# Kernel optimization log

Measured on AMD Instinct MI355X. Metric: run time of the kernel, lower is better.

## Reference

```python
import jax, jax.numpy as jnp
import numpy as np

N = 100_000      # nodes
E = 500_000      # bonds
DN = 128         # dim_node_embedding
DB = 64          # dim_bond_embedding
NTOK = 4         # num_bond_token
DIN = 2 * DN + 2 * DB  # 384
LEAKY = 0.001
LN_EPS = 1e-5
DIST_MAX = 20.0
STEP = 0.5


def _lrelu(v):
    return jnp.where(v >= 0, v, LEAKY * v)


def _layernorm(v, w, b):
    m = v.mean(-1, keepdims=True)
    var = ((v - m) ** 2).mean(-1, keepdims=True)
    return (v - m) / jnp.sqrt(var + LN_EPS) * w + b


def setup_inputs() -> dict:
    key = jax.random.key(0)
    ks = jax.random.split(key, 20)
    x = jax.random.normal(ks[0], (N, 3), dtype=jnp.float32) * 3.0
    pos = jax.random.normal(ks[1], (N, 3), dtype=jnp.float32)
    node_embedding = jax.random.normal(ks[2], (N, DN), dtype=jnp.float32)
    i0 = jax.random.randint(ks[3], (E,), 0, N)
    off = jax.random.randint(ks[4], (E,), 1, N)  # nonzero -> no self-bonds
    bond_index = jnp.stack([i0, (i0 + off) % N], axis=1).astype(jnp.int32)
    bond_types = jax.random.randint(ks[5], (E,), 0, NTOK).astype(jnp.int32)
    s = 0.02
    params = dict(
        bond_emb=jax.random.normal(ks[6], (NTOK, DB), dtype=jnp.float32),
        W0=jax.random.normal(ks[7], (DIN, DN), dtype=jnp.float32) * s,
        b0=jnp.zeros((DN,), jnp.float32),
        W1=jax.random.normal(ks[8], (DN, DN), dtype=jnp.float32) * s,
        b1=jnp.zeros((DN,), jnp.float32),
        ln1_w=jnp.ones((DN,), jnp.float32),
        ln1_b=jnp.zeros((DN,), jnp.float32),
        W2=jax.random.normal(ks[9], (DN, DN), dtype=jnp.float32) * s,
        b2=jnp.zeros((DN,), jnp.float32),
        ln2_w=jnp.ones((DN,), jnp.float32),
        ln2_b=jnp.zeros((DN,), jnp.float32),
        Wo=jax.random.normal(ks[10], (DN, 2), dtype=jnp.float32) * s,
        bo=jnp.zeros((2,), jnp.float32),
    )
    return dict(x=x, pos=pos, node_embedding=node_embedding,
                bond_index=bond_index, bond_types=bond_types, **params)


def reference(x, pos, node_embedding, bond_index, bond_types,
              bond_emb, W0, b0, W1, b1, ln1_w, ln1_b,
              W2, b2, ln2_w, ln2_b, Wo, bo):
    i = bond_index[:, 0]
    j = bond_index[:, 1]

    # ---- BondLength geometry ----
    diff = x[i] - x[j]                                   # [E,3]
    dist = jnp.linalg.norm(diff, axis=-1, keepdims=True)  # [E,1]
    u = diff / dist                                       # [E,3] unit j->i? (i-j)/d
    direction = jnp.stack([u, -u], axis=-1)               # [E,3,2]

    # ---- Smearing (gaussian RBF + overflow bin, normalized) ----
    offset = jnp.linspace(0.0, DIST_MAX, DB - 1, dtype=jnp.float32)  # [63]
    delta = DIST_MAX / (DB - 2)
    coeff = -0.5 / (delta * delta)
    rbf = jnp.exp(coeff * (dist - offset) ** 2)            # [E,63]
    ovf = (dist >= DIST_MAX).astype(x.dtype)               # [E,1]
    smear = jnp.concatenate([rbf, ovf], axis=-1)           # [E,64]
    smear = smear / smear.sum(axis=-1, keepdims=True)

    # ---- Edge MLP (LeakyMLP, num_layer=2, dim_end=2) ----
    feat = jnp.concatenate(
        [node_embedding[i], node_embedding[j], bond_emb[bond_types], smear],
        axis=-1)                                           # [E,384]
    h = _lrelu(feat @ W0 + b0)
    h = _lrelu(_layernorm(h @ W1 + b1, ln1_w, ln1_b))
    h = _lrelu(_layernorm(h @ W2 + b2, ln2_w, ln2_b))
    force = h @ Wo + bo                                    # [E,2]

    # ---- position update (scatter-add) ----
    update = force[:, None, :] * direction                 # [E,3,2]
    pos = pos.at[i].add(STEP * update[..., 0])
    pos = pos.at[j].add(STEP * update[..., 1])
    return pos
```

## Files before the change

kernel.cpp:

```cpp
#include <hip/hip_runtime.h>
#include <stdint.h>

#define N_EDGES 500000
#define N_NODES 100000
#define PREP_NG 2
#define TBINS 1280

typedef __attribute__((ext_vector_type(8))) short short8;
typedef __attribute__((ext_vector_type(4))) float floatx4;
typedef __attribute__((ext_vector_type(2))) float f32x2;

__device__ __forceinline__ uint16_t f2bf(float f) {
  union { float f; uint32_t u; } cv; cv.f = f;
  uint32_t u = cv.u;
  return (uint16_t)((u + 0x7FFFu + ((u >> 16) & 1u)) >> 16);
}
__device__ __forceinline__ uint32_t pk2bf(float lo, float hi) {
  return __builtin_amdgcn_perm(__float_as_uint(hi), __float_as_uint(lo), 0x07060302u);
}
__device__ __forceinline__ uint16_t bftrunc(float f) {
  return (uint16_t)(__float_as_uint(f) >> 16);
}
__device__ __forceinline__ float lrelu(float v) { return fmaxf(v, 0.001f * v); }

__device__ __forceinline__ f32x2 unpk2(uint32_t u) {
  return (f32x2){ __uint_as_float(u << 16), __uint_as_float(u & 0xFFFF0000u) };
}
__device__ __forceinline__ uint32_t comp2(uint32_t a, uint32_t b, uint32_t t0, uint32_t t1,
                                          f32x2 w2) {
  f32x2 p  = unpk2(a) + unpk2(b);
  f32x2 v0 = unpk2(t0), v1 = unpk2(t1);
  f32x2 r  = p + (v0 + w2 * (v1 - v0));
  f32x2 rl = r * 0.001f;
  return pk2bf(fmaxf(r.x, rl.x), fmaxf(r.y, rl.y));
}
__device__ __forceinline__ floatx4 lrelu4(floatx4 v) {
  floatx4 w = v * 0.001f;
  v.x = fmaxf(v.x, w.x); v.y = fmaxf(v.y, w.y);
  v.z = fmaxf(v.z, w.z); v.w = fmaxf(v.w, w.w);
  return v;
}

__global__ void prep0_kernel(const float* __restrict__ W0, const float* __restrict__ b0,
                             const float* __restrict__ W1, const float* __restrict__ W2,
                             const float* __restrict__ bemb,
                             uint16_t* __restrict__ w0ab, uint16_t* __restrict__ w1f,
                             uint16_t* __restrict__ w2f, float* __restrict__ be0f,
                             const float* __restrict__ pos, float* __restrict__ out, int npos) {
  int id = blockIdx.x * 256 + threadIdx.x;
  if (id < 32768) {
    int f = id;
    int j = f & 7, lane = (f >> 3) & 63, ntt = (f >> 9) & 15, ks = f >> 13;
    int k = ks * 32 + (lane >> 4) * 8 + j;
    int row = (ntt < 8) ? k : (128 + k);
    int col = (ntt & 7) * 16 + (lane & 15);
    w0ab[f] = f2bf(W0[row * 128 + col]);
  } else if (id < 49152) {
    int f = id - 32768;
    int j = f & 7, lane = (f >> 3) & 63, nt = (f >> 9) & 7, ks = f >> 12;
    int k = ks * 32 + (lane >> 4) * 8 + j;
    w1f[f] = f2bf(W1[k * 128 + nt * 16 + (lane & 15)]);
  } else if (id < 65536) {
    int f = id - 49152;
    int j = f & 7, lane = (f >> 3) & 63, nt = (f >> 9) & 7, ks = f >> 12;
    int k = ks * 32 + (lane >> 4) * 8 + j;
    w2f[f] = f2bf(W2[k * 128 + nt * 16 + (lane & 15)]);
  } else if (id < 66048) {
    int t = id - 65536; int ty = t >> 7, n = t & 127;
    float s = b0[n];
    for (int kk = 0; kk < 64; ++kk) s += bemb[ty * 64 + kk] * W0[(256 + kk) * 128 + n];
    be0f[t] = s;
  } else if (id - 66048 < npos) {
    out[id - 66048] = pos[id - 66048];
  }
}

__global__ __attribute__((amdgpu_flat_work_group_size(256, 256)))
void prep_tp_kernel(const float* __restrict__ W0, const float* __restrict__ be0f,
                    uint16_t* __restrict__ T,
                    const float* __restrict__ nemb, const uint16_t* __restrict__ w0ab,
                    uint16_t* __restrict__ Pa, uint16_t* __restrict__ Pb) {
  __shared__ __align__(16) uint16_t aLds[4 * PREP_NG * 16 * 136];
  __shared__ __align__(16) uint16_t sS[4][16][72];
  __shared__ float rbf[64];
  const int tid = threadIdx.x;

  if (blockIdx.x < TBINS) {
    int b = blockIdx.x;
    float dist = (float)b * (1.0f / 32.0f);
    const float delta = 20.0f / 62.0f;
    const float coeff = -0.5f / (delta * delta);
    if (tid < 64) {
      float v;
      if (tid < 63) { float d = dist - (float)tid * delta; v = __expf(coeff * d * d); }
      else v = (dist >= 20.0f) ? 1.0f : 0.0f;
      rbf[tid] = v;
    }
    __syncthreads();
    float sum = 0.0f;
    for (int k = 0; k < 64; ++k) sum += rbf[k];
    float rs = 1.0f / sum;
    for (int o = tid; o < 512; o += 256) {
      int ty = o >> 7, n = o & 127;
      float s = be0f[ty * 128 + n];
      for (int k = 0; k < 64; ++k) s += rbf[k] * rs * W0[(320 + k) * 128 + n];
      T[((size_t)(ty * TBINS + b)) * 128 + n] = f2bf(s);
    }
    return;
  }

  const int pblk = blockIdx.x - TBINS;
  const int lane = tid & 63;
  const int wave = tid >> 6;
  const int n15 = lane & 15;
  const int quad = lane >> 4;
  uint16_t* myA = aLds + wave * (PREP_NG * 16 * 136);
  const int base = pblk * (64 * PREP_NG) + wave * (16 * PREP_NG);

  {
    const int le = lane >> 2, sub = lane & 3;
#pragma unroll
    for (int it = 0; it < PREP_NG; ++it) {
      int r = base + it * 16 + le; if (r >= N_NODES) r = N_NODES - 1;
      const float4* src = (const float4*)(nemb + (size_t)r * 128);
#pragma unroll
      for (int g = 0; g < 4; ++g) {
        float4 a = src[sub * 8 + g * 2], b = src[sub * 8 + g * 2 + 1];
        uint4 pk;
        pk.x = pk2bf(a.x, a.y); pk.y = pk2bf(a.z, a.w);
        pk.z = pk2bf(b.x, b.y); pk.w = pk2bf(b.z, b.w);
        *(uint4*)(myA + (it * 16 + le) * 136 + sub * 32 + g * 8) = pk;
      }
    }
  }

  const short8* wfv = (const short8*)w0ab + lane;
  const int srow = lane >> 2, sch = lane & 3;
#pragma unroll
  for (int q = 0; q < 4; ++q) {
    short8 bfr[16];
#pragma unroll
    for (int ks = 0; ks < 4; ++ks)
#pragma unroll
      for (int nq = 0; nq < 4; ++nq)
        bfr[ks * 4 + nq] = wfv[(ks * 16 + q * 4 + nq) * 64];
    uint16_t* dst = (q < 2) ? Pa : Pb;
    const int cbase = (q & 1) * 64;
#pragma unroll
    for (int it = 0; it < PREP_NG; ++it) {
      floatx4 acc[4];
#pragma unroll
      for (int nq = 0; nq < 4; ++nq) acc[nq] = (floatx4){0.f, 0.f, 0.f, 0.f};
#pragma unroll
      for (int ks = 0; ks < 4; ++ks) {
        short8 a = *(const short8*)(myA + (it * 16 + n15) * 136 + ks * 32 + quad * 8);
#pragma unroll
        for (int nq = 0; nq < 4; ++nq)
          acc[nq] = __builtin_amdgcn_mfma_f32_16x16x32_bf16(a, bfr[ks * 4 + nq], acc[nq], 0, 0, 0);
      }
#pragma unroll
      for (int nq = 0; nq < 4; ++nq)
#pragma unroll
        for (int r = 0; r < 4; ++r)
          sS[wave][quad * 4 + r][nq * 16 + n15] = bftrunc(acc[nq][r]);
      int grow = base + it * 16 + srow;
      if (grow < N_NODES) {
        uint16_t* drow = dst + (size_t)grow * 128 + cbase;
#pragma unroll
        for (int h = 0; h < 2; ++h)
          *(uint4*)(drow + (h * 4 + sch) * 8) =
              *(const uint4*)&sS[wave][srow][(h * 4 + sch) * 8];
      }
    }
  }
}

__device__ __forceinline__ void gemm_g2(const uint16_t* __restrict__ wf,
                                        const uint16_t* aRow0, const uint16_t* aRow1,
                                        int lane, floatx4* acc0, floatx4* acc1) {
  short8 a0[4], a1[4];
#pragma unroll
  for (int ks = 0; ks < 4; ++ks) {
    a0[ks] = *(const short8*)(aRow0 + ks * 32);
    a1[ks] = *(const short8*)(aRow1 + ks * 32);
  }
  const short8* wv = (const short8*)wf + lane;
#pragma unroll
  for (int ks = 0; ks < 4; ++ks)
#pragma unroll
    for (int nt = 0; nt < 8; ++nt) {
      short8 b = wv[(ks * 8 + nt) * 64];
      acc0[nt] = __builtin_amdgcn_mfma_f32_16x16x32_bf16(a0[ks], b, acc0[nt], 0, 0, 0);
      acc1[nt] = __builtin_amdgcn_mfma_f32_16x16x32_bf16(a1[ks], b, acc1[nt], 0, 0, 0);
    }
}

__device__ __forceinline__ void epilogue1(floatx4* acc, uint16_t* hA, int n15, int quad,
                                          const float* __restrict__ b1,
                                          const float* __restrict__ ln1w,
                                          const float* __restrict__ ln1b) {
  float bv[8], wv[8], bb[8];
#pragma unroll
  for (int nt = 0; nt < 8; ++nt) {
    int col = nt * 16 + n15;
    bv[nt] = b1[col]; wv[nt] = ln1w[col]; bb[nt] = ln1b[col];
  }
  floatx4 s4 = {0.f, 0.f, 0.f, 0.f}, q4 = {0.f, 0.f, 0.f, 0.f};
#pragma unroll
  for (int nt = 0; nt < 8; ++nt) { floatx4 v = acc[nt] + bv[nt]; s4 += v; q4 += v * v; }
#pragma unroll
  for (int m = 1; m <= 8; m <<= 1) {
#pragma unroll
    for (int c = 0; c < 4; ++c) { s4[c] += __shfl_xor(s4[c], m); q4[c] += __shfl_xor(q4[c], m); }
  }
  floatx4 mean = s4 * (1.0f / 128.0f);
  floatx4 var = q4 * (1.0f / 128.0f) - mean * mean;
  floatx4 rstd;
  rstd.x = rsqrtf(var.x + 1e-5f); rstd.y = rsqrtf(var.y + 1e-5f);
  rstd.z = rsqrtf(var.z + 1e-5f); rstd.w = rsqrtf(var.w + 1e-5f);
#pragma unroll
  for (int nt = 0; nt < 8; ++nt) {
    floatx4 v = acc[nt] + bv[nt];
    floatx4 vn = lrelu4((v - mean) * (rstd * wv[nt]) + bb[nt]);
#pragma unroll
    for (int r = 0; r < 4; ++r)
      hA[(quad * 4 + r) * 136 + nt * 16 + n15] = bftrunc(vn[r]);
  }
}

__device__ __forceinline__ void epilogue2(floatx4* acc, int n15, int quad, int edge0, int gr0,
                                          const float (*u_lds)[3], const int (*ij_lds)[2],
                                          const float* __restrict__ b2,
                                          const float* __restrict__ ln2w,
                                          const float* __restrict__ ln2b,
                                          const float* __restrict__ Wo,
                                          const float* __restrict__ bo,
                                          float* __restrict__ out) {
  float bv[8], wv[8], bb[8], wo0[8], wo1[8];
#pragma unroll
  for (int nt = 0; nt < 8; ++nt) {
    int col = nt * 16 + n15;
    bv[nt] = b2[col]; wv[nt] = ln2w[col]; bb[nt] = ln2b[col];
    wo0[nt] = Wo[2 * col]; wo1[nt] = Wo[2 * col + 1];
  }
  floatx4 s4 = {0.f, 0.f, 0.f, 0.f}, q4 = {0.f, 0.f, 0.f, 0.f};
#pragma unroll
  for (int nt = 0; nt < 8; ++nt) { floatx4 v = acc[nt] + bv[nt]; s4 += v; q4 += v * v; }
#pragma unroll
  for (int m = 1; m <= 8; m <<= 1) {
#pragma unroll
    for (int c = 0; c < 4; ++c) { s4[c] += __shfl_xor(s4[c], m); q4[c] += __shfl_xor(q4[c], m); }
  }
  floatx4 mean = s4 * (1.0f / 128.0f);
  floatx4 var = q4 * (1.0f / 128.0f) - mean * mean;
  floatx4 rstd;
  rstd.x = rsqrtf(var.x + 1e-5f); rstd.y = rsqrtf(var.y + 1e-5f);
  rstd.z = rsqrtf(var.z + 1e-5f); rstd.w = rsqrtf(var.w + 1e-5f);
  floatx4 f0 = {0.f, 0.f, 0.f, 0.f}, f1 = {0.f, 0.f, 0.f, 0.f};
#pragma unroll
  for (int nt = 0; nt < 8; ++nt) {
    floatx4 v = acc[nt] + bv[nt];
    floatx4 vn = lrelu4((v - mean) * (rstd * wv[nt]) + bb[nt]);
    f0 += vn * wo0[nt];
    f1 += vn * wo1[nt];
  }
#pragma unroll
  for (int m = 1; m <= 8; m <<= 1) {
#pragma unroll
    for (int c = 0; c < 4; ++c) { f0[c] += __shfl_xor(f0[c], m); f1[c] += __shfl_xor(f1[c], m); }
  }
  if (n15 < 4) {
    int gr = gr0 + quad * 4 + n15;
    int ge2 = edge0 + quad * 4 + n15;
    if (ge2 < N_EDGES) {
      float F0 = (n15 == 0) ? f0.x : (n15 == 1) ? f0.y : (n15 == 2) ? f0.z : f0.w;
      float F1 = (n15 == 0) ? f1.x : (n15 == 1) ? f1.y : (n15 == 2) ? f1.z : f1.w;
      F0 += bo[0]; F1 += bo[1];
      float ux = u_lds[gr][0], uy = u_lds[gr][1], uz = u_lds[gr][2];
      int ii = ij_lds[gr][0], jj = ij_lds[gr][1];
      float c0 = 0.5f * F0;
      float c1 = -0.5f * F1;
      atomicAdd(out + 3 * ii,     c0 * ux);
      atomicAdd(out + 3 * ii + 1, c0 * uy);
      atomicAdd(out + 3 * ii + 2, c0 * uz);
      atomicAdd(out + 3 * jj,     c1 * ux);
      atomicAdd(out + 3 * jj + 1, c1 * uy);
      atomicAdd(out + 3 * jj + 2, c1 * uz);
    }
  }
}

__global__ __attribute__((amdgpu_flat_work_group_size(256, 256), amdgpu_waves_per_eu(4)))
void bond_mlp_kernel(const float* __restrict__ x,
                     const int* __restrict__ bidx, const int* __restrict__ btyp,
                     const uint16_t* __restrict__ Pa, const uint16_t* __restrict__ Pb,
                     const uint16_t* __restrict__ Tt, const uint16_t* __restrict__ w1f,
                     const uint16_t* __restrict__ w2f,
                     const float* __restrict__ b1, const float* __restrict__ ln1w,
                     const float* __restrict__ ln1b,
                     const float* __restrict__ b2, const float* __restrict__ ln2w,
                     const float* __restrict__ ln2b,
                     const float* __restrict__ Wo, const float* __restrict__ bo,
                     float* __restrict__ out) {
  __shared__ __align__(16) uint16_t hA_all[8 * 16 * 136];
  __shared__ float u_lds[128][3];
  __shared__ int ij_lds[128][2];

  const int tid = threadIdx.x;
  const int lane = tid & 63;
  const int wave = tid >> 6;
  const int n15 = lane & 15;
  const int quad = lane >> 4;

  uint16_t* hA0 = hA_all + (wave * 2 + 0) * (16 * 136);
  uint16_t* hA1 = hA_all + (wave * 2 + 1) * (16 * 136);

#pragma unroll
  for (int g = 0; g < 2; ++g) {
    uint16_t* hA = (g == 0) ? hA0 : hA1;
    const int le = lane >> 2, sub = lane & 3;
    const int gr = wave * 32 + g * 16 + le;
    const int ge = blockIdx.x * 128 + gr;
    const bool valid = ge < N_EDGES;
    int vi = 0, vj = 0, bt = 0;
    if (valid) {
      int2 ij = *(const int2*)(bidx + 2 * ge);
      vi = ij.x; vj = ij.y;
      bt = btyp[ge];
    }
    float dx, dy, dz;
    if (valid) {
      dx = x[3 * vi]     - x[3 * vj];
      dy = x[3 * vi + 1] - x[3 * vj + 1];
      dz = x[3 * vi + 2] - x[3 * vj + 2];
    } else { dx = 1.0f; dy = 0.0f; dz = 0.0f; }
    float dist = sqrtf(dx * dx + dy * dy + dz * dz);
    float rinv = 1.0f / dist;
    if (sub == 0) {
      u_lds[gr][0] = dx * rinv; u_lds[gr][1] = dy * rinv; u_lds[gr][2] = dz * rinv;
      ij_lds[gr][0] = vi; ij_lds[gr][1] = vj;
    }
    float fb = fminf(dist, 39.5f) * 32.0f;
    int bi = (int)fb;
    float w = fb - (float)bi;
    f32x2 w2 = {w, w};
    const uint4* pa = (const uint4*)(Pa + (size_t)vi * 128 + sub * 32);
    const uint4* pb = (const uint4*)(Pb + (size_t)vj * 128 + sub * 32);
    const uint16_t* trow = Tt + ((size_t)(bt * TBINS + bi)) * 128 + sub * 32;
    const uint4* t0p = (const uint4*)trow;
    const uint4* t1p = (const uint4*)(trow + 128);
#pragma unroll
    for (int gg = 0; gg < 4; ++gg) {
      uint4 av = pa[gg], bv = pb[gg], t0 = t0p[gg], t1 = t1p[gg];
      uint4 pk;
      pk.x = comp2(av.x, bv.x, t0.x, t1.x, w2);
      pk.y = comp2(av.y, bv.y, t0.y, t1.y, w2);
      pk.z = comp2(av.z, bv.z, t0.z, t1.z, w2);
      pk.w = comp2(av.w, bv.w, t0.w, t1.w, w2);
      *(uint4*)(hA + le * 136 + sub * 32 + gg * 8) = pk;
    }
  }

  const uint16_t* aRow0 = hA0 + n15 * 136 + quad * 8;
  const uint16_t* aRow1 = hA1 + n15 * 136 + quad * 8;

  floatx4 acc0[8], acc1[8];
#pragma unroll
  for (int nt = 0; nt < 8; ++nt) {
    acc0[nt] = (floatx4){0.f, 0.f, 0.f, 0.f};
    acc1[nt] = (floatx4){0.f, 0.f, 0.f, 0.f};
  }
  gemm_g2(w1f, aRow0, aRow1, lane, acc0, acc1);

  epilogue1(acc0, hA0, n15, quad, b1, ln1w, ln1b);
  epilogue1(acc1, hA1, n15, quad, b1, ln1w, ln1b);

#pragma unroll
  for (int nt = 0; nt < 8; ++nt) {
    acc0[nt] = (floatx4){0.f, 0.f, 0.f, 0.f};
    acc1[nt] = (floatx4){0.f, 0.f, 0.f, 0.f};
  }
  gemm_g2(w2f, aRow0, aRow1, lane, acc0, acc1);

  const int e0 = blockIdx.x * 128 + wave * 32;
  epilogue2(acc0, n15, quad, e0,      wave * 32,      u_lds, ij_lds, b2, ln2w, ln2b, Wo, bo, out);
  epilogue2(acc1, n15, quad, e0 + 16, wave * 32 + 16, u_lds, ij_lds, b2, ln2w, ln2b, Wo, bo, out);
}

extern "C" void kernel_launch(void* const* d_in, const int* in_sizes, int n_in,
                              void* d_out, int out_size, void* d_ws, size_t ws_size,
                              hipStream_t stream) {
  const float* x    = (const float*)d_in[0];
  const float* pos  = (const float*)d_in[1];
  const float* nemb = (const float*)d_in[2];
  const int*   bidx = (const int*)d_in[3];
  const int*   btyp = (const int*)d_in[4];
  const float* bemb = (const float*)d_in[5];
  const float* W0   = (const float*)d_in[6];
  const float* b0   = (const float*)d_in[7];
  const float* W1   = (const float*)d_in[8];
  const float* b1   = (const float*)d_in[9];
  const float* ln1w = (const float*)d_in[10];
  const float* ln1b = (const float*)d_in[11];
  const float* W2   = (const float*)d_in[12];
  const float* b2   = (const float*)d_in[13];
  const float* ln2w = (const float*)d_in[14];
  const float* ln2b = (const float*)d_in[15];
  const float* Wo   = (const float*)d_in[16];
  const float* bo   = (const float*)d_in[17];
  float* out = (float*)d_out;

  uint16_t* w0ab = (uint16_t*)d_ws;
  uint16_t* w1f  = w0ab + 32768;
  uint16_t* w2f  = w1f + 16384;
  float*    be0f = (float*)(w2f + 16384);
  uint16_t* Tt   = (uint16_t*)(be0f + 512);
  uint16_t* Pa   = Tt + (size_t)4 * TBINS * 128;
  uint16_t* Pb   = Pa + (size_t)N_NODES * 128;

  const int nblkP = (N_NODES + 64 * PREP_NG - 1) / (64 * PREP_NG);

  prep0_kernel<<<(66048 + out_size + 255) / 256, 256, 0, stream>>>(
      W0, b0, W1, W2, bemb, w0ab, w1f, w2f, be0f, pos, out, out_size);
  prep_tp_kernel<<<TBINS + nblkP, 256, 0, stream>>>(
      W0, be0f, Tt, nemb, w0ab, Pa, Pb);
  bond_mlp_kernel<<<(N_EDGES + 127) / 128, 256, 0, stream>>>(
      x, bidx, btyp, Pa, Pb, Tt, w1f, w2f,
      b1, ln1w, ln1b, b2, ln2w, ln2b, Wo, bo, out);
}
```

Baseline: 367.6 us.

## Process edge groups one at a time and batch gather loads before compute

The gather phase is moved into a helper that issues all node-embedding, table and position loads up front (position as a float3 load) before the interpolation math, which raises memory-level parallelism. The GEMMs now run on one 16-row group at a time with a single accumulator set instead of two interleaved ones, so fewer registers are live. Each weight fragment is then read twice from global/L2 instead of being shared across two MFMAs. The waves-per-EU hint drops from 4 to 3, which gives each wave more registers at the cost of fewer resident waves.

New measurement: 476.6 us. +29.6%, slower.

```diff
diff --git a/kernel.cpp b/kernel.cpp
--- a/kernel.cpp
+++ b/kernel.cpp
@@ -175,24 +175,76 @@
   }
 }
 
-__device__ __forceinline__ void gemm_g2(const uint16_t* __restrict__ wf,
-                                        const uint16_t* aRow0, const uint16_t* aRow1,
-                                        int lane, floatx4* acc0, floatx4* acc1) {
-  short8 a0[4], a1[4];
-#pragma unroll
-  for (int ks = 0; ks < 4; ++ks) {
-    a0[ks] = *(const short8*)(aRow0 + ks * 32);
-    a1[ks] = *(const short8*)(aRow1 + ks * 32);
-  }
+__device__ __forceinline__ void phase1(
+    int ge0, int gr0, int lane,
+    const float* __restrict__ x, const int* __restrict__ bidx,
+    const int* __restrict__ btyp,
+    const uint16_t* __restrict__ Pa, const uint16_t* __restrict__ Pb,
+    const uint16_t* __restrict__ Tt,
+    uint16_t* __restrict__ hA, float (*u_lds)[3], int (*ij_lds)[2]) {
+  const int le = lane >> 2, sub = lane & 3;
+  const int gr = gr0 + le;
+  const int ge = ge0 + le;
+  const bool valid = ge < N_EDGES;
+  int vi = 0, vj = 0, bt = 0;
+  if (valid) {
+    int2 ij = *(const int2*)(bidx + 2 * ge);
+    vi = ij.x; vj = ij.y;
+    bt = btyp[ge];
+  }
+  const uint4* pa = (const uint4*)(Pa + (size_t)vi * 128 + sub * 32);
+  const uint4* pb = (const uint4*)(Pb + (size_t)vj * 128 + sub * 32);
+  uint4 A[4], B[4];
+#pragma unroll
+  for (int g = 0; g < 4; ++g) A[g] = pa[g];
+#pragma unroll
+  for (int g = 0; g < 4; ++g) B[g] = pb[g];
+  float dx, dy, dz;
+  if (valid) {
+    float3 xi = *(const float3*)(x + 3 * vi);
+    float3 xj = *(const float3*)(x + 3 * vj);
+    dx = xi.x - xj.x; dy = xi.y - xj.y; dz = xi.z - xj.z;
+  } else { dx = 1.0f; dy = 0.0f; dz = 0.0f; }
+  float dist = sqrtf(dx * dx + dy * dy + dz * dz);
+  float rinv = 1.0f / dist;
+  if (sub == 0) {
+    u_lds[gr][0] = dx * rinv; u_lds[gr][1] = dy * rinv; u_lds[gr][2] = dz * rinv;
+    ij_lds[gr][0] = vi; ij_lds[gr][1] = vj;
+  }
+  float fb = fminf(dist, 39.5f) * 32.0f;
+  int bi = (int)fb;
+  float w = fb - (float)bi;
+  f32x2 w2 = {w, w};
+  const uint16_t* trow = Tt + ((size_t)(bt * TBINS + bi)) * 128 + sub * 32;
+  const uint4* t0p = (const uint4*)trow;
+  const uint4* t1p = (const uint4*)(trow + 128);
+  uint4 T0[4], T1[4];
+#pragma unroll
+  for (int g = 0; g < 4; ++g) T0[g] = t0p[g];
+#pragma unroll
+  for (int g = 0; g < 4; ++g) T1[g] = t1p[g];
+#pragma unroll
+  for (int g = 0; g < 4; ++g) {
+    uint4 pk;
+    pk.x = comp2(A[g].x, B[g].x, T0[g].x, T1[g].x, w2);
+    pk.y = comp2(A[g].y, B[g].y, T0[g].y, T1[g].y, w2);
+    pk.z = comp2(A[g].z, B[g].z, T0[g].z, T1[g].z, w2);
+    pk.w = comp2(A[g].w, B[g].w, T0[g].w, T1[g].w, w2);
+    *(uint4*)(hA + le * 136 + sub * 32 + g * 8) = pk;
+  }
+}
+
+__device__ __forceinline__ void gemm_g(const uint16_t* __restrict__ wf, const uint16_t* aRow,
+                                       int lane, floatx4* acc) {
+  short8 a[4];
+#pragma unroll
+  for (int ks = 0; ks < 4; ++ks) a[ks] = *(const short8*)(aRow + ks * 32);
   const short8* wv = (const short8*)wf + lane;
 #pragma unroll
   for (int ks = 0; ks < 4; ++ks)
 #pragma unroll
-    for (int nt = 0; nt < 8; ++nt) {
-      short8 b = wv[(ks * 8 + nt) * 64];
-      acc0[nt] = __builtin_amdgcn_mfma_f32_16x16x32_bf16(a0[ks], b, acc0[nt], 0, 0, 0);
-      acc1[nt] = __builtin_amdgcn_mfma_f32_16x16x32_bf16(a1[ks], b, acc1[nt], 0, 0, 0);
-    }
+    for (int nt = 0; nt < 8; ++nt)
+      acc[nt] = __builtin_amdgcn_mfma_f32_16x16x32_bf16(a[ks], wv[(ks * 8 + nt) * 64], acc[nt], 0, 0, 0);
 }
 
 __device__ __forceinline__ void epilogue1(floatx4* acc, uint16_t* hA, int n15, int quad,
@@ -290,7 +342,7 @@
   }
 }
 
-__global__ __attribute__((amdgpu_flat_work_group_size(256, 256), amdgpu_waves_per_eu(4)))
+__global__ __attribute__((amdgpu_flat_work_group_size(256, 256), amdgpu_waves_per_eu(3)))
 void bond_mlp_kernel(const float* __restrict__ x,
                      const int* __restrict__ bidx, const int* __restrict__ btyp,
                      const uint16_t* __restrict__ Pa, const uint16_t* __restrict__ Pb,
@@ -315,76 +367,36 @@
   uint16_t* hA0 = hA_all + (wave * 2 + 0) * (16 * 136);
   uint16_t* hA1 = hA_all + (wave * 2 + 1) * (16 * 136);
 
-#pragma unroll
-  for (int g = 0; g < 2; ++g) {
-    uint16_t* hA = (g == 0) ? hA0 : hA1;
-    const int le = lane >> 2, sub = lane & 3;
-    const int gr = wave * 32 + g * 16 + le;
-    const int ge = blockIdx.x * 128 + gr;
-    const bool valid = ge < N_EDGES;
-    int vi = 0, vj = 0, bt = 0;
-    if (valid) {
-      int2 ij = *(const int2*)(bidx + 2 * ge);
-      vi = ij.x; vj = ij.y;
-      bt = btyp[ge];
-    }
-    float dx, dy, dz;
-    if (valid) {
-      dx = x[3 * vi]     - x[3 * vj];
-      dy = x[3 * vi + 1] - x[3 * vj + 1];
-      dz = x[3 * vi + 2] - x[3 * vj + 2];
-    } else { dx = 1.0f; dy = 0.0f; dz = 0.0f; }
-    float dist = sqrtf(dx * dx + dy * dy + dz * dz);
-    float rinv = 1.0f / dist;
-    if (sub == 0) {
-      u_lds[gr][0] = dx * rinv; u_lds[gr][1] = dy * rinv; u_lds[gr][2] = dz * rinv;
-      ij_lds[gr][0] = vi; ij_lds[gr][1] = vj;
-    }
-    float fb = fminf(dist, 39.5f) * 32.0f;
-    int bi = (int)fb;
-    float w = fb - (float)bi;
-    f32x2 w2 = {w, w};
-    const uint4* pa = (const uint4*)(Pa + (size_t)vi * 128 + sub * 32);
-    const uint4* pb = (const uint4*)(Pb + (size_t)vj * 128 + sub * 32);
-    const uint16_t* trow = Tt + ((size_t)(bt * TBINS + bi)) * 128 + sub * 32;
-    const uint4* t0p = (const uint4*)trow;
-    const uint4* t1p = (const uint4*)(trow + 128);
-#pragma unroll
-    for (int gg = 0; gg < 4; ++gg) {
-      uint4 av = pa[gg], bv = pb[gg], t0 = t0p[gg], t1 = t1p[gg];
-      uint4 pk;
-      pk.x = comp2(av.x, bv.x, t0.x, t1.x, w2);
-      pk.y = comp2(av.y, bv.y, t0.y, t1.y, w2);
-      pk.z = comp2(av.z, bv.z, t0.z, t1.z, w2);
-      pk.w = comp2(av.w, bv.w, t0.w, t1.w, w2);
-      *(uint4*)(hA + le * 136 + sub * 32 + gg * 8) = pk;
-    }
-  }
+  const int e0 = blockIdx.x * 128 + wave * 32;
+  const int r0 = wave * 32;
+
+  phase1(e0,      r0,      lane, x, bidx, btyp, Pa, Pb, Tt, hA0, u_lds, ij_lds);
+  phase1(e0 + 16, r0 + 16, lane, x, bidx, btyp, Pa, Pb, Tt, hA1, u_lds, ij_lds);
 
   const uint16_t* aRow0 = hA0 + n15 * 136 + quad * 8;
   const uint16_t* aRow1 = hA1 + n15 * 136 + quad * 8;
 
-  floatx4 acc0[8], acc1[8];
-#pragma unroll
-  for (int nt = 0; nt < 8; ++nt) {
-    acc0[nt] = (floatx4){0.f, 0.f, 0.f, 0.f};
-    acc1[nt] = (floatx4){0.f, 0.f, 0.f, 0.f};
-  }
-  gemm_g2(w1f, aRow0, aRow1, lane, acc0, acc1);
-
-  epilogue1(acc0, hA0, n15, quad, b1, ln1w, ln1b);
-  epilogue1(acc1, hA1, n15, quad, b1, ln1w, ln1b);
-
-#pragma unroll
-  for (int nt = 0; nt < 8; ++nt) {
-    acc0[nt] = (floatx4){0.f, 0.f, 0.f, 0.f};
-    acc1[nt] = (floatx4){0.f, 0.f, 0.f, 0.f};
-  }
-  gemm_g2(w2f, aRow0, aRow1, lane, acc0, acc1);
-
-  const int e0 = blockIdx.x * 128 + wave * 32;
-  epilogue2(acc0, n15, quad, e0,      wave * 32,      u_lds, ij_lds, b2, ln2w, ln2b, Wo, bo, out);
-  epilogue2(acc1, n15, quad, e0 + 16, wave * 32 + 16, u_lds, ij_lds, b2, ln2w, ln2b, Wo, bo, out);
+  floatx4 acc[8];
+
+#pragma unroll
+  for (int nt = 0; nt < 8; ++nt) acc[nt] = (floatx4){0.f, 0.f, 0.f, 0.f};
+  gemm_g(w1f, aRow0, lane, acc);
+  epilogue1(acc, hA0, n15, quad, b1, ln1w, ln1b);
+
+#pragma unroll
+  for (int nt = 0; nt < 8; ++nt) acc[nt] = (floatx4){0.f, 0.f, 0.f, 0.f};
+  gemm_g(w1f, aRow1, lane, acc);
+  epilogue1(acc, hA1, n15, quad, b1, ln1w, ln1b);
+
+#pragma unroll
+  for (int nt = 0; nt < 8; ++nt) acc[nt] = (floatx4){0.f, 0.f, 0.f, 0.f};
+  gemm_g(w2f, aRow0, lane, acc);
+  epilogue2(acc, n15, quad, e0, r0, u_lds, ij_lds, b2, ln2w, ln2b, Wo, bo, out);
+
+#pragma unroll
+  for (int nt = 0; nt < 8; ++nt) acc[nt] = (floatx4){0.f, 0.f, 0.f, 0.f};
+  gemm_g(w2f, aRow1, lane, acc);
+  epilogue2(acc, n15, quad, e0 + 16, r0 + 16, u_lds, ij_lds, b2, ln2w, ln2b, Wo, bo, out);
 }
 
 extern "C" void kernel_launch(void* const* d_in, const int* in_sizes, int n_in,
```
